# Optimization experiments

Hardware: AMD Instinct MI355X
Metric: run time of the kernel (lower is better)

## Reference

```python
import jax, jax.numpy as jnp
import numpy as np
from jax import lax

T, D, H, O = 16384, 257, 512, 257


def setup_inputs() -> dict:
    key = jax.random.key(0)
    ks = jax.random.split(key, 7)
    s = 1.0 / np.sqrt(H)  # PyTorch LSTM/Linear uniform init scale
    u = lambda k, shp: jax.random.uniform(k, shp, jnp.float32, -s, s)
    return {
        "stft": jax.random.normal(ks[0], (T, D), jnp.float32),
        "W_ih": u(ks[1], (4 * H, D)),
        "W_hh": u(ks[2], (4 * H, H)),
        "b_ih": u(ks[3], (4 * H,)),
        "b_hh": u(ks[4], (4 * H,)),
        "W_out": u(ks[5], (O, H)),
        "b_out": u(ks[6], (O,)),
    }


def reference(stft, W_ih, W_hh, b_ih, b_hh, W_out, b_out):
    # Batch size is 1 (stft.view(T, 1, -1)), so we scan over [T, D] directly.
    # Precompute input-to-gate GEMM for all timesteps: [T, 4H]
    x_gates = stft @ W_ih.T + (b_ih + b_hh)

    def step(carry, xg):
        h, c = carry  # [H], [H]
        g = xg + h @ W_hh.T  # [4H], PyTorch gate order: i, f, g, o
        i, f, gg, o = jnp.split(g, 4)
        i = jax.nn.sigmoid(i)
        f = jax.nn.sigmoid(f)
        gg = jnp.tanh(gg)
        o = jax.nn.sigmoid(o)
        c = f * c + i * gg
        h = o * jnp.tanh(c)
        return (h, c), h

    h0 = jnp.zeros((H,), stft.dtype)  # init_hidden(): zeros
    c0 = jnp.zeros((H,), stft.dtype)
    _, hs = lax.scan(step, (h0, c0), x_gates)  # hs: [T, H]

    out_space = hs @ W_out.T + b_out  # [T, O]
    return jax.nn.log_softmax(out_space, axis=1)
```

## Files before the change

kernel.cpp:

```cpp
#include <hip/hip_runtime.h>
#include <cmath>

#define T_STEPS 16384
#define D_IN    257
#define H_DIM   512
#define O_DIM   257
#define G4      2048

typedef unsigned long long u64;

#define WS_XG_OFF     8192
#define WS_HS_OFF     (8192 + (size_t)T_STEPS * G4 * 4)

__device__ inline float fast_sigmoid(float x) {
    return 1.f / (1.f + __expf(-x));
}
__device__ inline float fast_tanh(float x) {
    float ax = fminf(fabsf(x), 15.f);
    float e  = __expf(2.f * ax);
    float t  = (e - 1.f) / (e + 1.f);
    return copysignf(t, x);
}
__device__ inline float dot4(float4 a, float4 b) {
    return a.x * b.x + a.y * b.y + a.z * b.z + a.w * b.w;
}

#define PIN4(v) asm volatile("" : "+v"(v.x), "+v"(v.y), "+v"(v.z), "+v"(v.w))

__global__ __launch_bounds__(256) void xgate_gemm(
    const float* __restrict__ stft, const float* __restrict__ W_ih,
    const float* __restrict__ b_ih, const float* __restrict__ b_hh,
    float* __restrict__ xg)
{
    const int tid = threadIdx.x;
    const int tx = tid & 15, ty = tid >> 4;
    const int j0 = blockIdx.x * 64;
    const int t0 = blockIdx.y * 64;

    __shared__ float s_a[64][17];
    __shared__ float s_b[64][17];

    float acc[4][4] = {};

    for (int k0 = 0; k0 < D_IN; k0 += 16) {
        #pragma unroll
        for (int l = 0; l < 4; ++l) {
            int idx = tid + l * 256;
            int r  = idx >> 4;
            int kk = idx & 15;
            int k  = k0 + kk;
            s_a[r][kk] = (k < D_IN) ? stft[(size_t)(t0 + r) * D_IN + k] : 0.f;
            s_b[r][kk] = (k < D_IN) ? W_ih[(size_t)(j0 + r) * D_IN + k] : 0.f;
        }
        __syncthreads();
        #pragma unroll
        for (int kk = 0; kk < 16; ++kk) {
            float a[4], b[4];
            #pragma unroll
            for (int r = 0; r < 4; ++r) a[r] = s_a[ty * 4 + r][kk];
            #pragma unroll
            for (int c = 0; c < 4; ++c) b[c] = s_b[tx * 4 + c][kk];
            #pragma unroll
            for (int r = 0; r < 4; ++r)
                #pragma unroll
                for (int c = 0; c < 4; ++c)
                    acc[r][c] += a[r] * b[c];
        }
        __syncthreads();
    }

    float bias[4];
    #pragma unroll
    for (int c = 0; c < 4; ++c) {
        int j = j0 + tx * 4 + c;
        bias[c] = b_ih[j] + b_hh[j];
    }
    #pragma unroll
    for (int r = 0; r < 4; ++r) {
        int t = t0 + ty * 4 + r;
        #pragma unroll
        for (int c = 0; c < 4; ++c) {
            xg[(size_t)t * G4 + j0 + tx * 4 + c] = acc[r][c] + bias[c];
        }
    }
}

__global__ __launch_bounds__(512, 1) void lstm_seq(
    const float* __restrict__ W_hh, const float* __restrict__ xg,
    float* __restrict__ hs, u64* __restrict__ msg)
{
    const int tid  = threadIdx.x;
    const int g    = blockIdx.x;
    const int w    = tid >> 6;
    const int lane = tid & 63;
    const int j    = lane >> 2;
    const int c    = lane & 3;
    const int colb = w * 64 + c * 16;

    const float* wbase = W_hh + (size_t)(g * 16 + j) * H_DIM + colb;
    const size_t gstride = (size_t)H_DIM * H_DIM;
    float4 wA0, wA1, wA2, wA3, wB0, wB1, wB2, wB3;
    float4 wC0, wC1, wC2, wC3, wD0, wD1, wD2, wD3;
    {
        const float4* p0 = (const float4*)(wbase);
        const float4* p1 = (const float4*)(wbase + gstride);
        const float4* p2 = (const float4*)(wbase + 2 * gstride);
        const float4* p3 = (const float4*)(wbase + 3 * gstride);
        wA0 = p0[0]; wA1 = p0[1]; wA2 = p0[2]; wA3 = p0[3];
        wB0 = p1[0]; wB1 = p1[1]; wB2 = p1[2]; wB3 = p1[3];
        wC0 = p2[0]; wC1 = p2[1]; wC2 = p2[2]; wC3 = p2[3];
        wD0 = p3[0]; wD1 = p3[1]; wD2 = p3[2]; wD3 = p3[3];
    }
    PIN4(wA0); PIN4(wA1); PIN4(wA2); PIN4(wA3);
    PIN4(wB0); PIN4(wB1); PIN4(wB2); PIN4(wB3);
    PIN4(wC0); PIN4(wC1); PIN4(wC2); PIN4(wC3);
    PIN4(wD0); PIN4(wD1); PIN4(wD2); PIN4(wD3);

    __shared__ float s_h[512];
    __shared__ float s_part[2][512];

    u64* slot0 = msg;
    u64* slot1 = msg + 512;

    float c_state = 0.f;
    const int t_j = lane & 15;

    for (int t = 0; t < T_STEPS; ++t) {
        const unsigned tagt = (unsigned)t;
        const int buf = t & 1;

        float xv = 0.f;
        if (w == 0)
            xv = __builtin_nontemporal_load(
                xg + (size_t)t * G4 + (lane >> 4) * H_DIM + g * 16 + t_j);

        u64* rp = (buf ? slot1 : slot0) + tid;
        u64 u;
        for (;;) {
            u = __hip_atomic_load(rp, __ATOMIC_RELAXED, __HIP_MEMORY_SCOPE_AGENT);
            if ((unsigned)(u >> 32) == tagt) break;
        }

        s_h[tid] = __uint_as_float((unsigned)u);

        const float4* hv = (const float4*)(s_h + colb);
        float4 h0 = hv[0], h1 = hv[1], h2 = hv[2], h3 = hv[3];

        float p0 = dot4(wA0, h0) + dot4(wA1, h1) + dot4(wA2, h2) + dot4(wA3, h3);
        float p1 = dot4(wB0, h0) + dot4(wB1, h1) + dot4(wB2, h2) + dot4(wB3, h3);
        float p2 = dot4(wC0, h0) + dot4(wC1, h1) + dot4(wC2, h2) + dot4(wC3, h3);
        float p3 = dot4(wD0, h0) + dot4(wD1, h1) + dot4(wD2, h2) + dot4(wD3, h3);

        const bool lo2 = (c < 2);
        float a0 = (lo2 ? p0 : p2) + __shfl_xor(lo2 ? p2 : p0, 2, 64);
        float a1 = (lo2 ? p1 : p3) + __shfl_xor(lo2 ? p3 : p1, 2, 64);
        const bool ev = ((c & 1) == 0);
        float fin = (ev ? a0 : a1) + __shfl_xor(ev ? a1 : a0, 1, 64);

        s_part[buf][w * 64 + c * 16 + j] = fin;

        asm volatile("s_waitcnt lgkmcnt(0)\n\ts_barrier" ::: "memory");

        if (w == 0) {
            const float* pp = &s_part[buf][0];
            float sum = xv;
            #pragma unroll
            for (int k = 0; k < 8; ++k) sum += pp[k * 64 + lane];

            float gi = __shfl(sum, t_j + 0,  64);
            float gf = __shfl(sum, t_j + 16, 64);
            float gg = __shfl(sum, t_j + 32, 64);
            float go = __shfl(sum, t_j + 48, 64);

            float iv = fast_sigmoid(gi);
            float fv = fast_sigmoid(gf);
            float ov = fast_sigmoid(go);
            float gv = fast_tanh(gg);
            c_state = fv * c_state + iv * gv;
            float hn = ov * fast_tanh(c_state);

            if (lane < 16) {
                __builtin_nontemporal_store(hn, hs + (size_t)t * H_DIM + g * 16 + lane);
                u64 m = ((u64)(tagt + 1) << 32) | (u64)__float_as_uint(hn);
                u64* wp = (((t + 1) & 1) ? slot1 : slot0) + (g * 16 + lane);
                __hip_atomic_store(wp, m, __ATOMIC_RELAXED, __HIP_MEMORY_SCOPE_AGENT);
            }
        }
    }
}

__global__ __launch_bounds__(256) void out_softmax(
    const float* __restrict__ hs, const float* __restrict__ W_out,
    const float* __restrict__ b_out, float* __restrict__ out)
{
    const int tid = threadIdx.x;
    const int t0  = blockIdx.x * 16;

    __shared__ float s_w[257 * 33];
    __shared__ float s_hs[16 * 33];
    __shared__ float s_o[16 * 257];
    __shared__ float s_red[8];

    float acc[16] = {};
    float acc256 = 0.f;

    for (int k0 = 0; k0 < H_DIM; k0 += 32) {
        for (int idx = tid; idx < 257 * 32; idx += 256) {
            int row = idx >> 5, col = idx & 31;
            s_w[row * 33 + col] = W_out[(size_t)row * H_DIM + k0 + col];
        }
        for (int idx = tid; idx < 16 * 32; idx += 256) {
            int row = idx >> 5, col = idx & 31;
            s_hs[row * 33 + col] = hs[(size_t)(t0 + row) * H_DIM + k0 + col];
        }
        __syncthreads();
        #pragma unroll
        for (int kk = 0; kk < 32; ++kk) {
            float w = s_w[tid * 33 + kk];
            #pragma unroll
            for (int r = 0; r < 16; ++r)
                acc[r] += s_hs[r * 33 + kk] * w;
        }
        if (tid < 16) {
            #pragma unroll
            for (int kk = 0; kk < 32; ++kk)
                acc256 += s_w[256 * 33 + kk] * s_hs[tid * 33 + kk];
        }
        __syncthreads();
    }

    float bias_c = b_out[tid];
    #pragma unroll
    for (int r = 0; r < 16; ++r) s_o[r * 257 + tid] = acc[r] + bias_c;
    if (tid < 16) s_o[tid * 257 + 256] = acc256 + b_out[256];
    __syncthreads();

    const int lane = tid & 63, wid = tid >> 6;
    for (int r = 0; r < 16; ++r) {
        float v  = s_o[r * 257 + tid];
        float vx = (tid == 0) ? s_o[r * 257 + 256] : -INFINITY;
        float m = fmaxf(v, vx);
        #pragma unroll
        for (int off = 32; off > 0; off >>= 1) m = fmaxf(m, __shfl_xor(m, off, 64));
        if (lane == 0) s_red[wid] = m;
        __syncthreads();
        m = fmaxf(fmaxf(s_red[0], s_red[1]), fmaxf(s_red[2], s_red[3]));
        float e = expf(v - m) + ((tid == 0) ? expf(vx - m) : 0.f);
        #pragma unroll
        for (int off = 32; off > 0; off >>= 1) e += __shfl_xor(e, off, 64);
        if (lane == 0) s_red[4 + wid] = e;
        __syncthreads();
        float s = s_red[4] + s_red[5] + s_red[6] + s_red[7];
        float lg = logf(s) + m;
        out[(size_t)(t0 + r) * O_DIM + tid] = v - lg;
        if (tid == 0) out[(size_t)(t0 + r) * O_DIM + 256] = vx - lg;
    }
}

extern "C" void kernel_launch(void* const* d_in, const int* in_sizes, int n_in,
                              void* d_out, int out_size, void* d_ws, size_t ws_size,
                              hipStream_t stream) {
    (void)in_sizes; (void)n_in; (void)out_size; (void)ws_size;

    const float* stft  = (const float*)d_in[0];
    const float* W_ih  = (const float*)d_in[1];
    const float* W_hh  = (const float*)d_in[2];
    const float* b_ih  = (const float*)d_in[3];
    const float* b_hh  = (const float*)d_in[4];
    const float* W_out = (const float*)d_in[5];
    const float* b_out = (const float*)d_in[6];
    float* out = (float*)d_out;

    char* ws = (char*)d_ws;
    u64* msg  = (u64*)ws;
    float* xg = (float*)(ws + WS_XG_OFF);
    float* hs = (float*)(ws + WS_HS_OFF);

    (void)hipMemsetAsync(ws, 0, 8192, stream);

    xgate_gemm<<<dim3(G4 / 64, T_STEPS / 64), 256, 0, stream>>>(
        stft, W_ih, b_ih, b_hh, xg);
    lstm_seq<<<32, 512, 0, stream>>>(W_hh, xg, hs, msg);
    out_softmax<<<T_STEPS / 16, 256, 0, stream>>>(hs, W_out, b_out, out);
}
```

Before: 24.70 ms.

## Enlarge xgate GEMM tiles, pipeline spin-wait loads, store h before hs

The input-gate GEMM moves from 64x64 to 128x128 tiles with 8x8 per-thread register blocking and a k-major shared layout read as float4, which raises arithmetic intensity per shared-memory load. The LSTM spin-wait now keeps several atomic loads in flight so a newly published value is seen sooner. The h message store is issued before the hs history store, putting the cross-block handoff first on the critical path. Total runtime is dominated by the sequential recurrence, so the GEMM change matters little. The larger tiles also raise register pressure and leave fewer blocks to fill the GPU.

```diff
diff --git a/kernel.cpp b/kernel.cpp
--- a/kernel.cpp
+++ b/kernel.cpp
@@ -26,6 +26,8 @@
 }
 
 #define PIN4(v) asm volatile("" : "+v"(v.x), "+v"(v.y), "+v"(v.z), "+v"(v.w))
+
+#define AL(p) __hip_atomic_load((p), __ATOMIC_RELAXED, __HIP_MEMORY_SCOPE_AGENT)
 
 __global__ __launch_bounds__(256) void xgate_gemm(
     const float* __restrict__ stft, const float* __restrict__ W_ih,
@@ -34,53 +36,54 @@
 {
     const int tid = threadIdx.x;
     const int tx = tid & 15, ty = tid >> 4;
-    const int j0 = blockIdx.x * 64;
-    const int t0 = blockIdx.y * 64;
-
-    __shared__ float s_a[64][17];
-    __shared__ float s_b[64][17];
-
-    float acc[4][4] = {};
+    const int j0 = blockIdx.x * 128;
+    const int t0 = blockIdx.y * 128;
+
+    __shared__ float s_a[16][132];
+    __shared__ float s_b[16][132];
+
+    float acc[8][8] = {};
 
     for (int k0 = 0; k0 < D_IN; k0 += 16) {
         #pragma unroll
-        for (int l = 0; l < 4; ++l) {
+        for (int l = 0; l < 8; ++l) {
             int idx = tid + l * 256;
-            int r  = idx >> 4;
-            int kk = idx & 15;
-            int k  = k0 + kk;
-            s_a[r][kk] = (k < D_IN) ? stft[(size_t)(t0 + r) * D_IN + k] : 0.f;
-            s_b[r][kk] = (k < D_IN) ? W_ih[(size_t)(j0 + r) * D_IN + k] : 0.f;
+            int r   = idx >> 4;
+            int kk  = idx & 15;
+            int k   = k0 + kk;
+            s_a[kk][r] = (k < D_IN) ? stft[(size_t)(t0 + r) * D_IN + k] : 0.f;
+            s_b[kk][r] = (k < D_IN) ? W_ih[(size_t)(j0 + r) * D_IN + k] : 0.f;
         }
         __syncthreads();
         #pragma unroll
         for (int kk = 0; kk < 16; ++kk) {
-            float a[4], b[4];
-            #pragma unroll
-            for (int r = 0; r < 4; ++r) a[r] = s_a[ty * 4 + r][kk];
-            #pragma unroll
-            for (int c = 0; c < 4; ++c) b[c] = s_b[tx * 4 + c][kk];
-            #pragma unroll
-            for (int r = 0; r < 4; ++r)
+            const float4* pa = (const float4*)&s_a[kk][ty * 8];
+            const float4* pb = (const float4*)&s_b[kk][tx * 8];
+            float4 a0 = pa[0], a1 = pa[1];
+            float4 b0 = pb[0], b1 = pb[1];
+            float ar[8] = {a0.x, a0.y, a0.z, a0.w, a1.x, a1.y, a1.z, a1.w};
+            float br[8] = {b0.x, b0.y, b0.z, b0.w, b1.x, b1.y, b1.z, b1.w};
+            #pragma unroll
+            for (int r = 0; r < 8; ++r)
                 #pragma unroll
-                for (int c = 0; c < 4; ++c)
-                    acc[r][c] += a[r] * b[c];
-        }
-        __syncthreads();
-    }
-
-    float bias[4];
+                for (int c = 0; c < 8; ++c)
+                    acc[r][c] += ar[r] * br[c];
+        }
+        __syncthreads();
+    }
+
+    float bias[8];
     #pragma unroll
-    for (int c = 0; c < 4; ++c) {
-        int j = j0 + tx * 4 + c;
+    for (int c = 0; c < 8; ++c) {
+        int j = j0 + tx * 8 + c;
         bias[c] = b_ih[j] + b_hh[j];
     }
     #pragma unroll
-    for (int r = 0; r < 4; ++r) {
-        int t = t0 + ty * 4 + r;
-        #pragma unroll
-        for (int c = 0; c < 4; ++c) {
-            xg[(size_t)t * G4 + j0 + tx * 4 + c] = acc[r][c] + bias[c];
+    for (int r = 0; r < 8; ++r) {
+        int t = t0 + ty * 8 + r;
+        #pragma unroll
+        for (int c = 0; c < 8; ++c) {
+            xg[(size_t)t * G4 + j0 + tx * 8 + c] = acc[r][c] + bias[c];
         }
     }
 }
@@ -136,9 +139,18 @@
 
         u64* rp = (buf ? slot1 : slot0) + tid;
         u64 u;
-        for (;;) {
-            u = __hip_atomic_load(rp, __ATOMIC_RELAXED, __HIP_MEMORY_SCOPE_AGENT);
-            if ((unsigned)(u >> 32) == tagt) break;
+        {
+            u64 p0 = AL(rp), p1 = AL(rp), p2 = AL(rp);
+            for (;;) {
+                u64 p3 = AL(rp);
+                if ((unsigned)(p0 >> 32) == tagt) { u = p0; break; }
+                p0 = AL(rp);
+                if ((unsigned)(p1 >> 32) == tagt) { u = p1; break; }
+                p1 = AL(rp);
+                if ((unsigned)(p2 >> 32) == tagt) { u = p2; break; }
+                p2 = AL(rp);
+                if ((unsigned)(p3 >> 32) == tagt) { u = p3; break; }
+            }
         }
 
         s_h[tid] = __uint_as_float((unsigned)u);
@@ -180,10 +192,10 @@
             float hn = ov * fast_tanh(c_state);
 
             if (lane < 16) {
-                __builtin_nontemporal_store(hn, hs + (size_t)t * H_DIM + g * 16 + lane);
                 u64 m = ((u64)(tagt + 1) << 32) | (u64)__float_as_uint(hn);
                 u64* wp = (((t + 1) & 1) ? slot1 : slot0) + (g * 16 + lane);
                 __hip_atomic_store(wp, m, __ATOMIC_RELAXED, __HIP_MEMORY_SCOPE_AGENT);
+                __builtin_nontemporal_store(hn, hs + (size_t)t * H_DIM + g * 16 + lane);
             }
         }
     }
@@ -278,7 +290,7 @@
 
     (void)hipMemsetAsync(ws, 0, 8192, stream);
 
-    xgate_gemm<<<dim3(G4 / 64, T_STEPS / 64), 256, 0, stream>>>(
+    xgate_gemm<<<dim3(G4 / 128, T_STEPS / 128), 256, 0, stream>>>(
         stft, W_ih, b_ih, b_hh, xg);
     lstm_seq<<<32, 512, 0, stream>>>(W_hh, xg, hs, msg);
     out_softmax<<<T_STEPS / 16, 256, 0, stream>>>(hs, W_out, b_out, out);
```

Measured after the change: 28.41 ms. +15.1%, slower.
